# Optimization experiments

Hardware: AMD Instinct MI355X
Metric: run time of the kernel (lower is better)

Reference implementation:

```python
import jax, jax.numpy as jnp
import numpy as np

M = 6           # Anderson memory slots (init default)
THRESHOLD = 30  # max forward iterations (forward default)
LAM = 1e-4      # Tikhonov regularization lambda
BETA = 1.0      # learn_beta=False -> beta=1.0 every step


def setup_inputs() -> dict:
    key = jax.random.key(0)
    k1, k2, k3 = jax.random.split(key, 3)
    bsz, d = 2048, 2048
    x0 = jax.random.normal(k1, (bsz, d), jnp.float32)
    # f(x) = tanh(x @ W + b): a contraction-ish layer standing in for the user-supplied f
    W = jax.random.normal(k2, (d, d), jnp.float32) * 0.02
    b = jax.random.normal(k3, (d,), jnp.float32)
    return {"x0": x0, "W": W, "b": b}


def reference(x0, W, b):
    def f(x):
        return jnp.tanh(x @ W + b)

    bsz, d = x0.shape
    m, threshold, lam, beta = M, THRESHOLD, LAM, BETA

    # Eval-mode circular buffers of size m (self.training == False branch)
    X = jnp.zeros((bsz, m, d), x0.dtype).at[:, 0].set(x0)
    F = jnp.zeros((bsz, m, d), x0.dtype).at[:, 0].set(f(x0))
    # torch: F = F.detach(); X = X.detach() (initial entries carry no grad)
    X = jax.lax.stop_gradient(X)
    F = jax.lax.stop_gradient(F)

    # x0 is random nonzero -> (x0 == 0).all() is False -> k_start = 1
    abs_trace, rel_trace = [], []
    eye_m = jnp.eye(m, dtype=x0.dtype)
    up = 0
    for k in range(1, threshold):  # fixed-count unrolled loop; n is static per step
        n = min(k, m)
        up = k % m
        G = F[:, :n] - X[:, :n]                                  # [bsz, n, d]
        GGt = jnp.einsum('bnd,bmd->bnm', G, G) + lam * eye_m[:n, :n]
        # Bordered system H: [[0, 1^T], [1, GG^T + lam I]], y = e_0
        H = (jnp.zeros((bsz, n + 1, n + 1), x0.dtype)
             .at[:, 0, 1:].set(1.0)
             .at[:, 1:, 0].set(1.0)
             .at[:, 1:, 1:].set(GGt))
        y = jnp.zeros((bsz, n + 1, 1), x0.dtype).at[:, 0, 0].set(1.0)
        alpha = jnp.linalg.solve(H, y)[:, 1:, 0]                 # [bsz, n]
        xnew = (beta * jnp.einsum('bn,bnd->bd', alpha, F[:, :n])
                + (1.0 - beta) * jnp.einsum('bn,bnd->bd', alpha, X[:, :n]))
        fnew = f(xnew)
        X = X.at[:, up].set(xnew)
        F = F.at[:, up].set(fnew)
        gx = fnew - xnew
        abs_diff = jnp.linalg.norm(gx)
        rel_diff = abs_diff / (1e-5 + jnp.linalg.norm(fnew))
        abs_trace.append(abs_diff)
        rel_trace.append(rel_diff)

    result = X[:, up]  # 'result' in the torch dict
    rel = jnp.stack(rel_trace).reshape(1, -1)
    absd = jnp.stack(abs_trace).reshape(1, -1)
    return result, X, rel, absd
```

## Files before the change

### kernel.cpp

```cpp
#include <hip/hip_runtime.h>
#include <math.h>

#define BSZ 2048
#define DIM 2048
#define MS 6
#define NIT 29
#define LAMREG 1e-4f
#define XROWS (MS*DIM)
#define N2 ((size_t)BSZ*DIM)

typedef __bf16 bf16x8 __attribute__((ext_vector_type(8)));
typedef __bf16 bf16x4 __attribute__((ext_vector_type(4)));
typedef float  f32x4  __attribute__((ext_vector_type(4)));

__device__ __forceinline__ void async16(const void* g, void* l) {
    __builtin_amdgcn_global_load_lds((const __attribute__((address_space(1))) void*)g,
                                     (__attribute__((address_space(3))) void*)l, 16, 0, 0);
}

__device__ __forceinline__ int swz(int r, int q) {
    return r * 32 + ((q ^ ((r >> 1) & 3)) << 3);
}

__global__ __launch_bounds__(256) void init_kernel(const float* __restrict__ x0,
                                                   float* __restrict__ Xout,
                                                   __bf16* __restrict__ Ahi,
                                                   __bf16* __restrict__ Alo,
                                                   float* __restrict__ norms) {
    int idx = blockIdx.x * 256 + threadIdx.x;
    if (idx < 16 * NIT) norms[idx] = 0.0f;
    for (int i = idx; i < BSZ * DIM; i += gridDim.x * 256) {
        int b = i >> 11;
        int j = i & (DIM - 1);
        float v = x0[i];
        Xout[(size_t)b * XROWS + j] = v;
        __bf16 h = (__bf16)v;
        Ahi[i] = h;
        Alo[i] = (__bf16)(v - (float)h);
    }
}

__global__ __launch_bounds__(256) void wt_split_kernel(const float* __restrict__ W,
                                                       __bf16* __restrict__ WThi,
                                                       __bf16* __restrict__ WTlo) {
    __shared__ float tile[32][33];
    const int tx = threadIdx.x & 31;
    const int ty = threadIdx.x >> 5;
    const int n0 = blockIdx.x * 32;
    const int k0 = blockIdx.y * 32;
#pragma unroll
    for (int i = 0; i < 32; i += 8)
        tile[ty + i][tx] = W[(size_t)(k0 + ty + i) * DIM + n0 + tx];
    __syncthreads();
#pragma unroll
    for (int i = 0; i < 32; i += 8) {
        float v = tile[tx][ty + i];
        __bf16 h = (__bf16)v;
        size_t o = (size_t)(n0 + ty + i) * DIM + k0 + tx;
        WThi[o] = h;
        WTlo[o] = (__bf16)(v - (float)h);
    }
}

__global__ __launch_bounds__(256, 2) void gemm_mfma_kernel(
    const __bf16* __restrict__ Ahi, const __bf16* __restrict__ Alo,
    const __bf16* __restrict__ WThi, const __bf16* __restrict__ WTlo,
    float* __restrict__ P)
{
    __shared__ __align__(16) __bf16 Ah[2][128 * 32];
    __shared__ __align__(16) __bf16 Al[2][128 * 32];
    __shared__ __align__(16) __bf16 Bh[2][128 * 32];
    __shared__ __align__(16) __bf16 Bl[2][128 * 32];

    const int id = blockIdx.x;
    const int xcd = id & 7;
    const int rest = id >> 3;
    const int ks = rest >> 5;
    const int slot = rest & 31;
    const int by = ((xcd & 3) << 2) | (slot & 3);
    const int bx = ((xcd >> 2) << 3) | (slot >> 2);
    const int m0 = by * 128;
    const int n0 = bx * 128;
    const int kbase = ks << 10;

    const int tid = threadIdx.x;
    const int l = tid & 63;
    const int w = tid >> 6;
    const int wm = (w & 1) * 64;
    const int wn = (w >> 1) * 64;
    const int rl = l & 15;
    const int quad = l >> 4;

    const int srow = w * 16 + (l >> 2);
    const int gchunk = (l & 3) ^ ((l >> 3) & 3);
    const int scol = gchunk << 3;
    const size_t aoff = (size_t)(m0 + srow) * DIM + kbase + scol;
    const size_t boff = (size_t)(n0 + srow) * DIM + kbase + scol;
    const int lo = w * 512;

    f32x4 acc[4][4];
#pragma unroll
    for (int t = 0; t < 4; t++)
#pragma unroll
        for (int u = 0; u < 4; u++) acc[t][u] = (f32x4){0.f, 0.f, 0.f, 0.f};

    auto stage = [&](int kb, int s) {
        async16(Ahi + aoff + kb, &Ah[s][lo]);
        async16(Ahi + aoff + (size_t)64 * DIM + kb, &Ah[s][lo + 2048]);
        async16(Alo + aoff + kb, &Al[s][lo]);
        async16(Alo + aoff + (size_t)64 * DIM + kb, &Al[s][lo + 2048]);
        async16(WThi + boff + kb, &Bh[s][lo]);
        async16(WThi + boff + (size_t)64 * DIM + kb, &Bh[s][lo + 2048]);
        async16(WTlo + boff + kb, &Bl[s][lo]);
        async16(WTlo + boff + (size_t)64 * DIM + kb, &Bl[s][lo + 2048]);
    };
    auto compute = [&](int s) {
        bf16x8 ah[4], al[4];
#pragma unroll
        for (int t = 0; t < 4; t++) {
            const int r = wm + t * 16 + rl;
            ah[t] = *(const bf16x8*)&Ah[s][swz(r, quad)];
            al[t] = *(const bf16x8*)&Al[s][swz(r, quad)];
        }
#pragma unroll
        for (int u = 0; u < 4; u++) {
            const int c = wn + u * 16 + rl;
            bf16x8 bh = *(const bf16x8*)&Bh[s][swz(c, quad)];
            bf16x8 bl = *(const bf16x8*)&Bl[s][swz(c, quad)];
#pragma unroll
            for (int t = 0; t < 4; t++) {
                acc[t][u] = __builtin_amdgcn_mfma_f32_16x16x32_bf16(ah[t], bh, acc[t][u], 0, 0, 0);
                acc[t][u] = __builtin_amdgcn_mfma_f32_16x16x32_bf16(al[t], bh, acc[t][u], 0, 0, 0);
                acc[t][u] = __builtin_amdgcn_mfma_f32_16x16x32_bf16(ah[t], bl, acc[t][u], 0, 0, 0);
            }
        }
    };

    stage(0, 0);
    for (int k0 = 0; k0 < 1024; k0 += 64) {
        __syncthreads();
        stage(k0 + 32, 1);
        compute(0);
        __syncthreads();
        if (k0 + 64 < 1024) stage(k0 + 64, 0);
        compute(1);
    }

    float* Pk = P + (size_t)ks * N2;
#pragma unroll
    for (int t = 0; t < 4; t++) {
#pragma unroll
        for (int r = 0; r < 4; r++) {
            const int row = m0 + wm + t * 16 + quad * 4 + r;
            float* pr = Pk + (size_t)row * DIM + n0 + wn;
#pragma unroll
            for (int u = 0; u < 4; u++) pr[u * 16 + rl] = acc[t][u][r];
        }
    }
}

__global__ __launch_bounds__(256) void mega_kernel(
    const float* __restrict__ P, const float* __restrict__ bias,
    float* __restrict__ Fb, float* __restrict__ Xb, float* __restrict__ Gb,
    float* __restrict__ GGt,
    __bf16* __restrict__ Ahi, __bf16* __restrict__ Alo,
    float* __restrict__ resultOrNull, float* __restrict__ normAcc,
    int up, int nact, int nxt)
{
    const int b = blockIdx.x;
    const int tid = threadIdx.x;
    const size_t rb = (size_t)b * XROWS;
    const size_t prow = (size_t)b * DIM;

    const f32x4* P0 = (const f32x4*)(P + prow);
    const f32x4* P1 = (const f32x4*)(P + N2 + prow);
    const f32x4* Bi = (const f32x4*)bias;
    const f32x4* Xu = (const f32x4*)(Xb + rb + (size_t)up * DIM);
    f32x4* Fu = (f32x4*)(Fb + rb + (size_t)up * DIM);
    f32x4* Gu = Gb ? (f32x4*)(Gb + rb + (size_t)up * DIM) : nullptr;

    f32x4 fv[2], gv[2];
    float s1 = 0.f, s2 = 0.f;
#pragma unroll
    for (int i = 0; i < 2; i++) {
        const int p4 = tid + 256 * i;
        f32x4 z = P0[p4] + P1[p4] + Bi[p4];
        f32x4 t;
        t.x = tanhf(z.x); t.y = tanhf(z.y); t.z = tanhf(z.z); t.w = tanhf(z.w);
        f32x4 xv = Xu[p4];
        f32x4 g = t - xv;
        fv[i] = t; gv[i] = g;
        Fu[p4] = t;
        if (Gu) Gu[p4] = g;
        s1 += g.x * g.x + g.y * g.y + g.z * g.z + g.w * g.w;
        s2 += t.x * t.x + t.y * t.y + t.z * t.z + t.w * t.w;
    }

    float acc[8];
#pragma unroll
    for (int p = 0; p < MS; p++) acc[p] = 0.f;
    acc[6] = s1; acc[7] = s2;

    if (nact > 0) {
#pragma unroll
        for (int j = 0; j < MS; j++) {
            if (j < nact) {
                if (j == up) { acc[j] = s1; continue; }
                float a = 0.f;
                if (Gb) {
                    const f32x4* Gj = (const f32x4*)(Gb + rb + (size_t)j * DIM);
#pragma unroll
                    for (int i = 0; i < 2; i++) {
                        const int p4 = tid + 256 * i;
                        f32x4 gj = Gj[p4];
                        a += gv[i].x * gj.x + gv[i].y * gj.y + gv[i].z * gj.z + gv[i].w * gj.w;
                    }
                } else {
                    const f32x4* Fj = (const f32x4*)(Fb + rb + (size_t)j * DIM);
                    const f32x4* Xj = (const f32x4*)(Xb + rb + (size_t)j * DIM);
#pragma unroll
                    for (int i = 0; i < 2; i++) {
                        const int p4 = tid + 256 * i;
                        f32x4 gj = Fj[p4] - Xj[p4];
                        a += gv[i].x * gj.x + gv[i].y * gj.y + gv[i].z * gj.z + gv[i].w * gj.w;
                    }
                }
                acc[j] = a;
            }
        }
    }

#pragma unroll
    for (int p = 0; p < 8; p++) {
        float v = acc[p];
#pragma unroll
        for (int off = 32; off > 0; off >>= 1) v += __shfl_down(v, off);
        acc[p] = v;
    }
    __shared__ float red[4][8];
    __shared__ float Hs[7][8];
    __shared__ float alf[7];
    const int lane = tid & 63, wave = tid >> 6;
    if (lane == 0) {
#pragma unroll
        for (int p = 0; p < 8; p++) red[wave][p] = acc[p];
    }
    __syncthreads();

    if (tid == 0) {
        float d[8];
#pragma unroll
        for (int p = 0; p < 8; p++)
            d[p] = red[0][p] + red[1][p] + red[2][p] + red[3][p];
        if (normAcc) {
            atomicAdd(&normAcc[b & 7], d[6]);
            atomicAdd(&normAcc[8 + (b & 7)], d[7]);
        }
        if (nact > 0) {
            float* gg = GGt + (size_t)b * 36;
            for (int j = 0; j < nact; j++) {
                gg[up * 6 + j] = d[j];
                gg[j * 6 + up] = d[j];
            }
            const int np = nact + 1;
            for (int i = 0; i < np; i++) {
                for (int j = 0; j < np; j++) {
                    float v;
                    if (i == 0 && j == 0) v = 0.0f;
                    else if (i == 0 || j == 0) v = 1.0f;
                    else {
                        v = gg[(i - 1) * 6 + (j - 1)];
                        if (i == j) v += LAMREG;
                    }
                    Hs[i][j] = v;
                }
                Hs[i][7] = (i == 0) ? 1.0f : 0.0f;
            }
            for (int c = 0; c < np; c++) {
                int piv = c;
                float mx = fabsf(Hs[c][c]);
                for (int r = c + 1; r < np; r++) {
                    float a = fabsf(Hs[r][c]);
                    if (a > mx) { mx = a; piv = r; }
                }
                if (piv != c) {
                    for (int cc = c; cc <= 7; cc++) {
                        float t = Hs[c][cc]; Hs[c][cc] = Hs[piv][cc]; Hs[piv][cc] = t;
                    }
                }
                float inv = 1.0f / Hs[c][c];
                for (int r = c + 1; r < np; r++) {
                    float f = Hs[r][c] * inv;
                    for (int cc = c; cc <= 7; cc++) Hs[r][cc] -= f * Hs[c][cc];
                }
            }
            float sol[7];
            for (int c = np - 1; c >= 0; c--) {
                float s = Hs[c][7];
                for (int cc = c + 1; cc < np; cc++) s -= Hs[c][cc] * sol[cc];
                sol[c] = s / Hs[c][c];
            }
            for (int i = 0; i < nact; i++) alf[i] = sol[i + 1];
        }
    }
    __syncthreads();

    if (nxt >= 0) {
        f32x4 s[2] = {(f32x4){0.f,0.f,0.f,0.f}, (f32x4){0.f,0.f,0.f,0.f}};
        for (int i2 = 0; i2 < nact; i2++) {
            const float a = alf[i2];
            if (i2 == up) {
#pragma unroll
                for (int i = 0; i < 2; i++) {
                    s[i].x = fmaf(a, fv[i].x, s[i].x);
                    s[i].y = fmaf(a, fv[i].y, s[i].y);
                    s[i].z = fmaf(a, fv[i].z, s[i].z);
                    s[i].w = fmaf(a, fv[i].w, s[i].w);
                }
            } else {
                const f32x4* Fi = (const f32x4*)(Fb + rb + (size_t)i2 * DIM);
#pragma unroll
                for (int i = 0; i < 2; i++) {
                    const int p4 = tid + 256 * i;
                    f32x4 fj = Fi[p4];
                    s[i].x = fmaf(a, fj.x, s[i].x);
                    s[i].y = fmaf(a, fj.y, s[i].y);
                    s[i].z = fmaf(a, fj.z, s[i].z);
                    s[i].w = fmaf(a, fj.w, s[i].w);
                }
            }
        }
        f32x4* Xn = (f32x4*)(Xb + rb + (size_t)nxt * DIM);
#pragma unroll
        for (int i = 0; i < 2; i++) {
            const int p4 = tid + 256 * i;
            Xn[p4] = s[i];
            if (resultOrNull) ((f32x4*)(resultOrNull + prow))[p4] = s[i];
            bf16x4 hh, ll;
#pragma unroll
            for (int c = 0; c < 4; c++) {
                float v = s[i][c];
                __bf16 h = (__bf16)v;
                hh[c] = h;
                ll[c] = (__bf16)(v - (float)h);
            }
            *(bf16x4*)&Ahi[prow + (size_t)p4 * 4] = hh;
            *(bf16x4*)&Alo[prow + (size_t)p4 * 4] = ll;
        }
    }
}

__global__ void finalize_kernel(const float* __restrict__ norms,
                                float* __restrict__ rel, float* __restrict__ absd)
{
    int t = threadIdx.x;
    if (t < NIT) {
        float a2 = 0.f, f2 = 0.f;
        for (int i = 0; i < 8; i++) {
            a2 += norms[t * 16 + i];
            f2 += norms[t * 16 + 8 + i];
        }
        float a = sqrtf(a2);
        absd[t] = a;
        rel[t] = a / (1e-5f + sqrtf(f2));
    }
}

extern "C" void kernel_launch(void* const* d_in, const int* in_sizes, int n_in,
                              void* d_out, int out_size, void* d_ws, size_t ws_size,
                              hipStream_t stream) {
    const float* x0   = (const float*)d_in[0];
    const float* W    = (const float*)d_in[1];
    const float* bias = (const float*)d_in[2];

    float* out    = (float*)d_out;
    float* result = out;
    float* Xout   = out + (size_t)BSZ * DIM;
    float* rel    = Xout + (size_t)BSZ * MS * DIM;
    float* absd   = rel + NIT;

    char* ws = (char*)d_ws;
    float* F     = (float*)ws;
    float* norms = F + (size_t)BSZ * MS * DIM;
    float* GGt   = norms + 512;
    float* P     = GGt + (size_t)BSZ * 36;
    char* p = (char*)(P + 2 * N2);
    size_t off = ((size_t)(p - ws) + 255) & ~(size_t)255;
    __bf16* Ahi  = (__bf16*)(ws + off);  off += (size_t)BSZ * DIM * 2;
    __bf16* Alo  = (__bf16*)(ws + off);  off += (size_t)BSZ * DIM * 2;
    __bf16* WThi = (__bf16*)(ws + off);  off += (size_t)DIM * DIM * 2;
    __bf16* WTlo = (__bf16*)(ws + off);  off += (size_t)DIM * DIM * 2;
    float* G = nullptr;
    if (ws_size >= off + (size_t)BSZ * MS * DIM * 4 + 256) {
        off = (off + 255) & ~(size_t)255;
        G = (float*)(ws + off);
    }

    wt_split_kernel<<<dim3(64, 64), 256, 0, stream>>>(W, WThi, WTlo);
    init_kernel<<<2048, 256, 0, stream>>>(x0, Xout, Ahi, Alo, norms);

    for (int j = 0; j <= NIT; j++) {
        gemm_mfma_kernel<<<512, 256, 0, stream>>>(Ahi, Alo, WThi, WTlo, P);
        int up   = j % MS;
        int nact = (j < NIT) ? ((j + 1 < MS) ? (j + 1) : MS) : 0;
        int nxt  = (j < NIT) ? ((j + 1) % MS) : -1;
        mega_kernel<<<BSZ, 256, 0, stream>>>(P, bias, F, Xout, G, GGt, Ahi, Alo,
                                             (j == NIT - 1) ? result : nullptr,
                                             (j >= 1) ? (norms + 16 * (j - 1)) : nullptr,
                                             up, nact, nxt);
    }
    finalize_kernel<<<1, 64, 0, stream>>>(norms, rel, absd);
}
```

Before: 4.587 ms.

## Map one wave per batch row and solve the Anderson system with wave shuffles

The per-row epilogue kernel now assigns a single 64-lane wave to each batch row instead of a 256-thread block, launching a quarter as many blocks. The GGt reductions use xor-shuffles only, with no shared memory or __syncthreads. The small bordered linear system is solved in parallel across lanes, one matrix row per lane, using shuffle-based partial pivoting, replacing the serial single-thread Gaussian elimination. This removes block barriers and serial solve latency, at the cost of more registers per thread (8 f32x4 of F and G held per lane) and more shuffle traffic.

```diff
diff --git a/kernel.cpp b/kernel.cpp
--- a/kernel.cpp
+++ b/kernel.cpp
@@ -20,6 +20,17 @@
 
 __device__ __forceinline__ int swz(int r, int q) {
     return r * 32 + ((q ^ ((r >> 1) & 3)) << 3);
+}
+
+__device__ __forceinline__ f32x4 fma4(float a, f32x4 x, f32x4 acc) {
+    acc.x = fmaf(a, x.x, acc.x);
+    acc.y = fmaf(a, x.y, acc.y);
+    acc.z = fmaf(a, x.z, acc.z);
+    acc.w = fmaf(a, x.w, acc.w);
+    return acc;
+}
+__device__ __forceinline__ float dot4(f32x4 a, f32x4 b) {
+    return a.x*b.x + a.y*b.y + a.z*b.z + a.w*b.w;
 }
 
 __global__ __launch_bounds__(256) void init_kernel(const float* __restrict__ x0,
@@ -167,8 +178,9 @@
     float* __restrict__ resultOrNull, float* __restrict__ normAcc,
     int up, int nact, int nxt)
 {
-    const int b = blockIdx.x;
-    const int tid = threadIdx.x;
+    const int wave = threadIdx.x >> 6;
+    const int l = threadIdx.x & 63;
+    const int b = blockIdx.x * 4 + wave;
     const size_t rb = (size_t)b * XROWS;
     const size_t prow = (size_t)b * DIM;
 
@@ -178,22 +190,31 @@
     const f32x4* Xu = (const f32x4*)(Xb + rb + (size_t)up * DIM);
     f32x4* Fu = (f32x4*)(Fb + rb + (size_t)up * DIM);
     f32x4* Gu = Gb ? (f32x4*)(Gb + rb + (size_t)up * DIM) : nullptr;
-
-    f32x4 fv[2], gv[2];
+    float* gg = GGt + (size_t)b * 36;
+
+    float grow[6];
+    {
+        const int a = l - 1;
+        const int aa = (a >= 0 && a < 6) ? a : 0;
+#pragma unroll
+        for (int c = 0; c < 6; c++) grow[c] = gg[aa * 6 + c];
+    }
+
+    f32x4 fv[8], gv[8];
     float s1 = 0.f, s2 = 0.f;
 #pragma unroll
-    for (int i = 0; i < 2; i++) {
-        const int p4 = tid + 256 * i;
-        f32x4 z = P0[p4] + P1[p4] + Bi[p4];
+    for (int c = 0; c < 8; c++) {
+        const int idx = l + 64 * c;
+        f32x4 z = P0[idx] + P1[idx] + Bi[idx];
         f32x4 t;
         t.x = tanhf(z.x); t.y = tanhf(z.y); t.z = tanhf(z.z); t.w = tanhf(z.w);
-        f32x4 xv = Xu[p4];
+        f32x4 xv = Xu[idx];
         f32x4 g = t - xv;
-        fv[i] = t; gv[i] = g;
-        Fu[p4] = t;
-        if (Gu) Gu[p4] = g;
-        s1 += g.x * g.x + g.y * g.y + g.z * g.z + g.w * g.w;
-        s2 += t.x * t.x + t.y * t.y + t.z * t.z + t.w * t.w;
+        fv[c] = t; gv[c] = g;
+        Fu[idx] = t;
+        if (Gu) Gu[idx] = g;
+        s1 += dot4(g, g);
+        s2 += dot4(t, t);
     }
 
     float acc[8];
@@ -201,151 +222,145 @@
     for (int p = 0; p < MS; p++) acc[p] = 0.f;
     acc[6] = s1; acc[7] = s2;
 
+    if (Gb) {
+#pragma unroll
+        for (int c = 0; c < 8; c++) {
+            const int idx = l + 64 * c;
+#pragma unroll
+            for (int j = 0; j < MS; j++) {
+                if (j < nact && j != up) {
+                    f32x4 gj = ((const f32x4*)(Gb + rb + (size_t)j * DIM))[idx];
+                    acc[j] += dot4(gv[c], gj);
+                }
+            }
+        }
+    } else {
+#pragma unroll
+        for (int c = 0; c < 8; c++) {
+            const int idx = l + 64 * c;
+#pragma unroll
+            for (int j = 0; j < MS; j++) {
+                if (j < nact && j != up) {
+                    f32x4 fj = ((const f32x4*)(Fb + rb + (size_t)j * DIM))[idx];
+                    f32x4 xj = ((const f32x4*)(Xb + rb + (size_t)j * DIM))[idx];
+                    acc[j] += dot4(gv[c], fj - xj);
+                }
+            }
+        }
+    }
+#pragma unroll
+    for (int j = 0; j < MS; j++)
+        if (j == up) acc[j] = s1;
+
+#pragma unroll
+    for (int p = 0; p < 8; p++) {
+        float v = acc[p];
+#pragma unroll
+        for (int off = 32; off > 0; off >>= 1) v += __shfl_xor(v, off);
+        acc[p] = v;
+    }
+
+    if (normAcc) {
+        if (l == 0) atomicAdd(&normAcc[b & 7], acc[6]);
+        if (l == 1) atomicAdd(&normAcc[8 + (b & 7)], acc[7]);
+    }
+
+    float sol[7];
+#pragma unroll
+    for (int p = 0; p < 7; p++) sol[p] = 0.f;
+
     if (nact > 0) {
-#pragma unroll
-        for (int j = 0; j < MS; j++) {
-            if (j < nact) {
-                if (j == up) { acc[j] = s1; continue; }
-                float a = 0.f;
-                if (Gb) {
-                    const f32x4* Gj = (const f32x4*)(Gb + rb + (size_t)j * DIM);
-#pragma unroll
-                    for (int i = 0; i < 2; i++) {
-                        const int p4 = tid + 256 * i;
-                        f32x4 gj = Gj[p4];
-                        a += gv[i].x * gj.x + gv[i].y * gj.y + gv[i].z * gj.z + gv[i].w * gj.w;
-                    }
-                } else {
-                    const f32x4* Fj = (const f32x4*)(Fb + rb + (size_t)j * DIM);
-                    const f32x4* Xj = (const f32x4*)(Xb + rb + (size_t)j * DIM);
-#pragma unroll
-                    for (int i = 0; i < 2; i++) {
-                        const int p4 = tid + 256 * i;
-                        f32x4 gj = Fj[p4] - Xj[p4];
-                        a += gv[i].x * gj.x + gv[i].y * gj.y + gv[i].z * gj.z + gv[i].w * gj.w;
+        const int a = l - 1;
+        float accl = (l == 0) ? acc[0] : (l == 1) ? acc[1] : (l == 2) ? acc[2]
+                   : (l == 3) ? acc[3] : (l == 4) ? acc[4] : (l == 5) ? acc[5] : 0.f;
+        float acca = (a == 0) ? acc[0] : (a == 1) ? acc[1] : (a == 2) ? acc[2]
+                   : (a == 3) ? acc[3] : (a == 4) ? acc[4] : (a == 5) ? acc[5] : 0.f;
+        if (l < nact) {
+            gg[up * 6 + l] = accl;
+            gg[l * 6 + up] = accl;
+        }
+        const int np = nact + 1;
+        float r[8];
+        {
+            const int i = l;
+            r[0] = (i == 0) ? 0.f : 1.f;
+#pragma unroll
+            for (int j = 1; j < 7; j++) {
+                const int c = j - 1;
+                float v;
+                if (i == 0) v = 1.f;
+                else v = (a == up) ? acc[c] : ((c == up) ? acca : grow[c]);
+                if (i == j) v += LAMREG;
+                r[j] = v;
+            }
+            r[7] = (i == 0) ? 1.f : 0.f;
+        }
+#pragma unroll
+        for (int c = 0; c < 7; c++) {
+            if (c < np) {
+                float key = (l >= c && l < np) ? fabsf(r[c]) : -1.f;
+                int idx = l;
+#pragma unroll
+                for (int off = 32; off > 0; off >>= 1) {
+                    float ok = __shfl_xor(key, off);
+                    int oi = __shfl_xor(idx, off);
+                    if (ok > key || (ok == key && oi < idx)) { key = ok; idx = oi; }
+                }
+                const int src = (l == c) ? idx : ((l == idx) ? c : l);
+#pragma unroll
+                for (int k = 0; k < 8; k++) r[k] = __shfl(r[k], src);
+                float pr[8];
+#pragma unroll
+                for (int k = 0; k < 8; k++) pr[k] = __shfl(r[k], c);
+                const float inv = 1.f / pr[c];
+                const float f = (l > c && l < np) ? r[c] * inv : 0.f;
+#pragma unroll
+                for (int k = 0; k < 8; k++) r[k] = fmaf(-f, pr[k], r[k]);
+            }
+        }
+#pragma unroll
+        for (int c = 6; c >= 0; c--) {
+            if (c < np) {
+                float s = r[7];
+#pragma unroll
+                for (int cc = 6; cc > 0; cc--)
+                    if (cc > c && cc < np) s = fmaf(-r[cc], sol[cc], s);
+                s /= r[c];
+                sol[c] = __shfl(s, c);
+            }
+        }
+    }
+
+    if (nxt >= 0) {
+        f32x4* Xn = (f32x4*)(Xb + rb + (size_t)nxt * DIM);
+#pragma unroll
+        for (int c = 0; c < 8; c++) {
+            const int idx = l + 64 * c;
+            f32x4 s = (f32x4){0.f, 0.f, 0.f, 0.f};
+#pragma unroll
+            for (int j = 0; j < MS; j++) {
+                if (j < nact) {
+                    const float a = sol[j + 1];
+                    if (j == up) {
+                        s = fma4(a, fv[c], s);
+                    } else {
+                        f32x4 fj = ((const f32x4*)(Fb + rb + (size_t)j * DIM))[idx];
+                        s = fma4(a, fj, s);
                     }
                 }
-                acc[j] = a;
-            }
-        }
-    }
-
-#pragma unroll
-    for (int p = 0; p < 8; p++) {
-        float v = acc[p];
-#pragma unroll
-        for (int off = 32; off > 0; off >>= 1) v += __shfl_down(v, off);
-        acc[p] = v;
-    }
-    __shared__ float red[4][8];
-    __shared__ float Hs[7][8];
-    __shared__ float alf[7];
-    const int lane = tid & 63, wave = tid >> 6;
-    if (lane == 0) {
-#pragma unroll
-        for (int p = 0; p < 8; p++) red[wave][p] = acc[p];
-    }
-    __syncthreads();
-
-    if (tid == 0) {
-        float d[8];
-#pragma unroll
-        for (int p = 0; p < 8; p++)
-            d[p] = red[0][p] + red[1][p] + red[2][p] + red[3][p];
-        if (normAcc) {
-            atomicAdd(&normAcc[b & 7], d[6]);
-            atomicAdd(&normAcc[8 + (b & 7)], d[7]);
-        }
-        if (nact > 0) {
-            float* gg = GGt + (size_t)b * 36;
-            for (int j = 0; j < nact; j++) {
-                gg[up * 6 + j] = d[j];
-                gg[j * 6 + up] = d[j];
-            }
-            const int np = nact + 1;
-            for (int i = 0; i < np; i++) {
-                for (int j = 0; j < np; j++) {
-                    float v;
-                    if (i == 0 && j == 0) v = 0.0f;
-                    else if (i == 0 || j == 0) v = 1.0f;
-                    else {
-                        v = gg[(i - 1) * 6 + (j - 1)];
-                        if (i == j) v += LAMREG;
-                    }
-                    Hs[i][j] = v;
-                }
-                Hs[i][7] = (i == 0) ? 1.0f : 0.0f;
-            }
-            for (int c = 0; c < np; c++) {
-                int piv = c;
-                float mx = fabsf(Hs[c][c]);
-                for (int r = c + 1; r < np; r++) {
-                    float a = fabsf(Hs[r][c]);
-                    if (a > mx) { mx = a; piv = r; }
-                }
-                if (piv != c) {
-                    for (int cc = c; cc <= 7; cc++) {
-                        float t = Hs[c][cc]; Hs[c][cc] = Hs[piv][cc]; Hs[piv][cc] = t;
-                    }
-                }
-                float inv = 1.0f / Hs[c][c];
-                for (int r = c + 1; r < np; r++) {
-                    float f = Hs[r][c] * inv;
-                    for (int cc = c; cc <= 7; cc++) Hs[r][cc] -= f * Hs[c][cc];
-                }
-            }
-            float sol[7];
-            for (int c = np - 1; c >= 0; c--) {
-                float s = Hs[c][7];
-                for (int cc = c + 1; cc < np; cc++) s -= Hs[c][cc] * sol[cc];
-                sol[c] = s / Hs[c][c];
-            }
-            for (int i = 0; i < nact; i++) alf[i] = sol[i + 1];
-        }
-    }
-    __syncthreads();
-
-    if (nxt >= 0) {
-        f32x4 s[2] = {(f32x4){0.f,0.f,0.f,0.f}, (f32x4){0.f,0.f,0.f,0.f}};
-        for (int i2 = 0; i2 < nact; i2++) {
-            const float a = alf[i2];
-            if (i2 == up) {
-#pragma unroll
-                for (int i = 0; i < 2; i++) {
-                    s[i].x = fmaf(a, fv[i].x, s[i].x);
-                    s[i].y = fmaf(a, fv[i].y, s[i].y);
-                    s[i].z = fmaf(a, fv[i].z, s[i].z);
-                    s[i].w = fmaf(a, fv[i].w, s[i].w);
-                }
-            } else {
-                const f32x4* Fi = (const f32x4*)(Fb + rb + (size_t)i2 * DIM);
-#pragma unroll
-                for (int i = 0; i < 2; i++) {
-                    const int p4 = tid + 256 * i;
-                    f32x4 fj = Fi[p4];
-                    s[i].x = fmaf(a, fj.x, s[i].x);
-                    s[i].y = fmaf(a, fj.y, s[i].y);
-                    s[i].z = fmaf(a, fj.z, s[i].z);
-                    s[i].w = fmaf(a, fj.w, s[i].w);
-                }
-            }
-        }
-        f32x4* Xn = (f32x4*)(Xb + rb + (size_t)nxt * DIM);
-#pragma unroll
-        for (int i = 0; i < 2; i++) {
-            const int p4 = tid + 256 * i;
-            Xn[p4] = s[i];
-            if (resultOrNull) ((f32x4*)(resultOrNull + prow))[p4] = s[i];
+            }
+            Xn[idx] = s;
+            if (resultOrNull) ((f32x4*)(resultOrNull + prow))[idx] = s;
             bf16x4 hh, ll;
 #pragma unroll
-            for (int c = 0; c < 4; c++) {
-                float v = s[i][c];
+            for (int q = 0; q < 4; q++) {
+                float v = s[q];
                 __bf16 h = (__bf16)v;
-                hh[c] = h;
-                ll[c] = (__bf16)(v - (float)h);
-            }
-            *(bf16x4*)&Ahi[prow + (size_t)p4 * 4] = hh;
-            *(bf16x4*)&Alo[prow + (size_t)p4 * 4] = ll;
+                hh[q] = h;
+                ll[q] = (__bf16)(v - (float)h);
+            }
+            *(bf16x4*)&Ahi[prow + (size_t)idx * 4] = hh;
+            *(bf16x4*)&Alo[prow + (size_t)idx * 4] = ll;
         }
     }
 }
@@ -404,10 +419,10 @@
         int up   = j % MS;
         int nact = (j < NIT) ? ((j + 1 < MS) ? (j + 1) : MS) : 0;
         int nxt  = (j < NIT) ? ((j + 1) % MS) : -1;
-        mega_kernel<<<BSZ, 256, 0, stream>>>(P, bias, F, Xout, G, GGt, Ahi, Alo,
-                                             (j == NIT - 1) ? result : nullptr,
-                                             (j >= 1) ? (norms + 16 * (j - 1)) : nullptr,
-                                             up, nact, nxt);
+        mega_kernel<<<BSZ / 4, 256, 0, stream>>>(P, bias, F, Xout, G, GGt, Ahi, Alo,
+                                                 (j == NIT - 1) ? result : nullptr,
+                                                 (j >= 1) ? (norms + 16 * (j - 1)) : nullptr,
+                                                 up, nact, nxt);
     }
     finalize_kernel<<<1, 64, 0, stream>>>(norms, rel, absd);
 }
```

New measurement: 4.857 ms. +5.9%, slower.
